# Performance work log

Hardware: AMD Instinct MI355X
Metric: run time of the kernel (lower is better)

## Reference

```python
import jax, jax.numpy as jnp
import numpy as np

N, E, G, D, H, L, IN = 50000, 800000, 16, 64, 4, 4, 7
NEG = 0.2       # LeakyReLU slope (module and GATv2 default)
EPS = 1e-5      # LayerNorm eps


def _lrelu(t):
    return jax.nn.leaky_relu(t, NEG)


def _ln(x, w, b):
    m = x.mean(-1, keepdims=True)
    v = ((x - m) ** 2).mean(-1, keepdims=True)
    return (x - m) * jax.lax.rsqrt(v + EPS) * w + b


def setup_inputs() -> dict:
    key = jax.random.key(0)
    ks = jax.random.split(key, 32)
    p = lambda i, shape: jax.random.normal(ks[i], shape, jnp.float32) * 0.05
    return dict(
        x=jax.random.normal(ks[0], (N, IN), jnp.float32),
        edge_attr=jax.random.normal(ks[1], (E, 3), jnp.float32),
        edge_index=jax.random.randint(ks[2], (2, E), 0, N),
        batch=jnp.sort(jax.random.randint(ks[3], (N,), 0, G)),
        enc_W=p(4, (IN, D)), enc_b=p(5, (D,)),
        Wl=p(6, (L, D, H * D)), bl=p(7, (L, H * D)),
        Wr=p(8, (L, D, H * D)), br=p(9, (L, H * D)),
        We=p(10, (L, 3, H * D)),
        att_w=p(11, (L, H, D)), gat_b=p(12, (L, D)),
        ln1_w=jnp.ones((L, D)), ln1_b=jnp.zeros((L, D)),
        ln2_w=jnp.ones((L, D)), ln2_b=jnp.zeros((L, D)),
        ffn_W1=p(13, (L, D, 2 * D)), ffn_b1=p(14, (L, 2 * D)),
        ffn_W2=p(15, (L, 2 * D, D)), ffn_b2=p(16, (L, D)),
        n2g_W1=p(17, (L, D, D)), n2g_b1=p(18, (L, D)),
        n2g_W2=p(19, (L, D, D)), n2g_b2=p(20, (L, D)),
        g2n_W=p(21, (L, 2 * D, D)), g2n_b=p(22, (L, D)),
        dec_W1=p(23, (D, D)), dec_b1=p(24, (D,)),
        dec_W2=p(25, (D, 2)), dec_b2=p(26, (2,)),
    )


def reference(x, edge_attr, edge_index, batch, enc_W, enc_b, Wl, bl, Wr, br, We,
              att_w, gat_b, ln1_w, ln1_b, ln2_w, ln2_b, ffn_W1, ffn_b1, ffn_W2,
              ffn_b2, n2g_W1, n2g_b1, n2g_W2, n2g_b2, g2n_W, g2n_b,
              dec_W1, dec_b1, dec_W2, dec_b2):
    # add self loops with mean edge_attr fill (PyG GATv2Conv default)
    loops = jnp.arange(N)
    src = jnp.concatenate([edge_index[0], loops])
    dst = jnp.concatenate([edge_index[1], loops])
    ea = jnp.concatenate([edge_attr, jnp.broadcast_to(edge_attr.mean(0), (N, 3))], 0)

    h = x @ enc_W + enc_b  # [N, D]
    for l in range(L):
        # ---- GATv2Conv (heads=H, concat=False -> mean over heads) ----
        xl = (h @ Wl[l] + bl[l]).reshape(N, H, D)   # source transform
        xr = (h @ Wr[l] + br[l]).reshape(N, H, D)   # target transform
        ee = (ea @ We[l]).reshape(-1, H, D)          # edge transform
        s = _lrelu(xl[src] + xr[dst] + ee)           # [Etot, H, D]
        logits = jnp.einsum('ehd,hd->eh', s, att_w[l])
        mx = jax.ops.segment_max(logits, dst, num_segments=N)
        ex = jnp.exp(logits - mx[dst])
        den = jax.ops.segment_sum(ex, dst, num_segments=N)
        alpha = ex / den[dst]                        # segment softmax per dst node
        agg = jax.ops.segment_sum(alpha[..., None] * xl[src], dst, num_segments=N)
        gat_out = agg.mean(1) + gat_b[l]             # [N, D]
        # ---- residual + LN + FFN + LN ----
        h = _ln(h + gat_out, ln1_w[l], ln1_b[l])
        h = _ln(h + _lrelu(h @ ffn_W1[l] + ffn_b1[l]) @ ffn_W2[l] + ffn_b2[l],
                ln2_w[l], ln2_b[l])
        # ---- GlobalContextLayer ----
        lat = _lrelu(h @ n2g_W1[l] + n2g_b1[l]) @ n2g_W2[l] + n2g_b2[l]
        cnt = jnp.maximum(jax.ops.segment_sum(jnp.ones((N,), h.dtype), batch,
                                              num_segments=G), 1.0)
        g_mean = jax.ops.segment_sum(lat, batch, num_segments=G) / cnt[:, None]
        g_max = jax.ops.segment_max(lat, batch, num_segments=G)
        gate = jax.nn.sigmoid(jnp.concatenate([g_mean, g_max], 1) @ g2n_W[l] + g2n_b[l])
        h = h * gate[batch]
    # ---- decoder ----
    return _lrelu(h @ dec_W1 + dec_b1) @ dec_W2 + dec_b2  # [N, 2]
```

## Files before the change

kernel.cpp:

```cpp
#include <hip/hip_runtime.h>

#define DEV __device__ __forceinline__

constexpr int Nn  = 50000;
constexpr int Ee  = 800000;
constexpr int Et  = 850000;
constexpr int Gg  = 16;
constexpr int Dd  = 64;
constexpr int Hh  = 4;
constexpr int Ll  = 4;
constexpr int INd = 7;
constexpr float NEG  = 0.2f;
constexpr float EPSL = 1e-5f;

DEV float lrelu(float x){ return fmaxf(x, NEG*x); }
DEV float wsum64(float v){
  v += __shfl_xor(v,1); v += __shfl_xor(v,2); v += __shfl_xor(v,4);
  v += __shfl_xor(v,8); v += __shfl_xor(v,16); v += __shfl_xor(v,32);
  return v;
}
DEV void atomicMaxF(float* a, float v){
  if (v >= 0.f) atomicMax((int*)a, __float_as_int(v));
  else          atomicMin((unsigned int*)a, __float_as_uint(v));
}
DEV unsigned short f2bf(float f){
  unsigned int u = __float_as_uint(f);
  unsigned int r = (u + 0x7FFFu + ((u >> 16) & 1u)) >> 16;
  return (unsigned short)r;
}
DEV float bf2f(unsigned short b){
  return __uint_as_float(((unsigned int)b) << 16);
}


__global__ void k_init(int* deg, float* g_sum, float* g_max, int* grp_cnt, float* ea_sum){
  int i = blockIdx.x*256 + threadIdx.x;
  if (i < Nn) deg[i] = 0;
  if (i < Gg*Dd){ g_sum[i] = 0.f; g_max[i] = -3.4e38f; }
  if (i < Gg) grp_cnt[i] = 0;
  if (i < 3) ea_sum[i] = 0.f;
}

__global__ void k_eamean(const float* __restrict__ ea, float* __restrict__ ea_sum){
  __shared__ float ps[4][3];
  int tid = threadIdx.x;
  float s0=0.f, s1=0.f, s2=0.f;
  int stride = gridDim.x * blockDim.x;
  for (int i = blockIdx.x*blockDim.x + tid; i < Ee; i += stride){
    s0 += ea[3*i]; s1 += ea[3*i+1]; s2 += ea[3*i+2];
  }
  s0 = wsum64(s0); s1 = wsum64(s1); s2 = wsum64(s2);
  int wid = tid >> 6;
  if ((tid & 63) == 0){ ps[wid][0]=s0; ps[wid][1]=s1; ps[wid][2]=s2; }
  __syncthreads();
  if (tid == 0){
    atomicAdd(ea_sum+0, ps[0][0]+ps[1][0]+ps[2][0]+ps[3][0]);
    atomicAdd(ea_sum+1, ps[0][1]+ps[1][1]+ps[2][1]+ps[3][1]);
    atomicAdd(ea_sum+2, ps[0][2]+ps[1][2]+ps[2][2]+ps[3][2]);
  }
}

__global__ void k_deg(const int* __restrict__ ei_dst, int* __restrict__ deg){
  int e = blockIdx.x*256 + threadIdx.x;
  if (e >= Et) return;
  int dst = (e < Ee) ? ei_dst[e] : (e - Ee);
  atomicAdd(&deg[dst], 1);
}

__global__ void k_bcnt(const int* __restrict__ batch, int* __restrict__ grp_cnt){
  __shared__ int c[Gg];
  if (threadIdx.x < Gg) c[threadIdx.x] = 0;
  __syncthreads();
  int i = blockIdx.x*256 + threadIdx.x;
  if (i < Nn) atomicAdd(&c[batch[i]], 1);
  __syncthreads();
  if (threadIdx.x < Gg && c[threadIdx.x]) atomicAdd(&grp_cnt[threadIdx.x], c[threadIdx.x]);
}

__global__ __launch_bounds__(1024) void k_scan(
    const int* __restrict__ deg, int* __restrict__ indptr, int* __restrict__ fill,
    const float* __restrict__ ea_sum, float* __restrict__ ea_mean)
{
  __shared__ int tot[1024];
  int tid = threadIdx.x;
  if (tid < 3) ea_mean[tid] = ea_sum[tid] * (1.f/(float)Ee);
  constexpr int CH = (Nn + 1023)/1024;
  int b0 = tid*CH;
  int loc[CH];
  int s = 0;
  #pragma unroll
  for (int i=0;i<CH;++i){
    int idx = b0+i;
    int d = (idx < Nn) ? deg[idx] : 0;
    loc[i] = s; s += d;
  }
  tot[tid] = s;
  __syncthreads();
  for (int off=1; off<1024; off<<=1){
    int v = (tid>=off) ? tot[tid-off] : 0;
    __syncthreads();
    tot[tid] += v;
    __syncthreads();
  }
  int base = (tid==0) ? 0 : tot[tid-1];
  #pragma unroll
  for (int i=0;i<CH;++i){
    int idx = b0+i;
    if (idx < Nn){
      int ex = base + loc[i];
      fill[idx] = ex;
      indptr[idx+1] = ex + deg[idx];
    }
  }
  if (tid==0) indptr[0] = 0;
}

__global__ void k_scatter(const int* __restrict__ ei_src, const int* __restrict__ ei_dst,
                          const float* __restrict__ ea, const float* __restrict__ ea_mean,
                          int* __restrict__ fill, float4* __restrict__ meta){
  int e = blockIdx.x*256 + threadIdx.x;
  if (e >= Et) return;
  int src, dst; float a0, a1, a2;
  if (e < Ee){
    src = ei_src[e]; dst = ei_dst[e];
    a0 = ea[3*e]; a1 = ea[3*e+1]; a2 = ea[3*e+2];
  } else {
    src = dst = e - Ee;
    a0 = ea_mean[0]; a1 = ea_mean[1]; a2 = ea_mean[2];
  }
  int pos = atomicAdd(&fill[dst], 1);
  meta[pos] = make_float4(__int_as_float(src), a0, a1, a2);
}

__global__ void k_tw(const float* __restrict__ fW1, const float* __restrict__ gW1,
                     float* __restrict__ fW1T, float* __restrict__ gW1T){
  int i = blockIdx.x*256 + threadIdx.x;
  if (i < Ll*64*128){
    int l = i >> 13, r = (i >> 7) & 63, c = i & 127;
    fW1T[l*8192 + c*64 + r] = fW1[i];
  }
  if (i < Ll*64*64){
    int l = i >> 12, r = (i >> 6) & 63, c = i & 63;
    gW1T[l*4096 + c*64 + r] = gW1[i];
  }
}


__global__ __launch_bounds__(256) void k_enc(
    const float* __restrict__ x, const float* __restrict__ W, const float* __restrict__ b,
    float* __restrict__ h)
{
  int i = blockIdx.x*256 + threadIdx.x;
  if (i >= Nn*Dd) return;
  int n = i >> 6, d = i & 63;
  float s = b[d];
  #pragma unroll
  for (int k=0;k<INd;++k) s = fmaf(x[n*INd+k], W[k*Dd+d], s);
  h[i] = s;
}


__global__ __launch_bounds__(256) void k_xlxr(
    float* __restrict__ h, const float* __restrict__ gate, const int* __restrict__ batch,
    const float* __restrict__ Wl, const float* __restrict__ bl,
    const float* __restrict__ Wr, const float* __restrict__ br,
    unsigned short* __restrict__ xlb, float* __restrict__ xr)
{
  __shared__ float lh[32*68];
  int tid = threadIdx.x;
  int n0 = blockIdx.x * 32;
  for (int r=0; r<8; ++r){
    int idx = r*256 + tid;
    int nl = idx >> 6, d = idx & 63;
    int node = n0 + nl;
    float v = 0.f;
    if (node < Nn){
      v = h[(size_t)node*64 + d];
      if (gate){ v *= gate[batch[node]*64 + d]; h[(size_t)node*64 + d] = v; }
    }
    lh[nl*68 + d] = v;
  }
  __syncthreads();
  int lane = tid & 63;
  int nb = (tid >> 6) * 8;
  int c0 = lane * 8;
  bool isXl = (c0 < 256);
  const float* W; const float* bb; int col;
  if (isXl){ W = Wl; bb = bl; col = c0; }
  else     { W = Wr; bb = br; col = c0 - 256; }
  float4 bA = *reinterpret_cast<const float4*>(bb + col);
  float4 bB = *reinterpret_cast<const float4*>(bb + col + 4);
  float acc[8][8];
  #pragma unroll
  for (int nq=0; nq<8; ++nq){
    acc[nq][0]=bA.x; acc[nq][1]=bA.y; acc[nq][2]=bA.z; acc[nq][3]=bA.w;
    acc[nq][4]=bB.x; acc[nq][5]=bB.y; acc[nq][6]=bB.z; acc[nq][7]=bB.w;
  }
  for (int d=0; d<64; d+=4){
    float4 wA[4], wB[4];
    #pragma unroll
    for (int dq=0; dq<4; ++dq){
      wA[dq] = *reinterpret_cast<const float4*>(W + (d+dq)*256 + col);
      wB[dq] = *reinterpret_cast<const float4*>(W + (d+dq)*256 + col + 4);
    }
    #pragma unroll
    for (int nq=0; nq<8; ++nq){
      float4 hv = *reinterpret_cast<const float4*>(&lh[(nb+nq)*68 + d]);
      #pragma unroll
      for (int dq=0; dq<4; ++dq){
        float hh = (dq==0)? hv.x : (dq==1)? hv.y : (dq==2)? hv.z : hv.w;
        acc[nq][0] = fmaf(hh, wA[dq].x, acc[nq][0]);
        acc[nq][1] = fmaf(hh, wA[dq].y, acc[nq][1]);
        acc[nq][2] = fmaf(hh, wA[dq].z, acc[nq][2]);
        acc[nq][3] = fmaf(hh, wA[dq].w, acc[nq][3]);
        acc[nq][4] = fmaf(hh, wB[dq].x, acc[nq][4]);
        acc[nq][5] = fmaf(hh, wB[dq].y, acc[nq][5]);
        acc[nq][6] = fmaf(hh, wB[dq].z, acc[nq][6]);
        acc[nq][7] = fmaf(hh, wB[dq].w, acc[nq][7]);
      }
    }
  }
  if (isXl){
    #pragma unroll
    for (int nq=0; nq<8; ++nq){
      int node = n0 + nb + nq;
      if (node < Nn){
        uint4 pk;
        pk.x = (unsigned int)f2bf(acc[nq][0]) | ((unsigned int)f2bf(acc[nq][1])<<16);
        pk.y = (unsigned int)f2bf(acc[nq][2]) | ((unsigned int)f2bf(acc[nq][3])<<16);
        pk.z = (unsigned int)f2bf(acc[nq][4]) | ((unsigned int)f2bf(acc[nq][5])<<16);
        pk.w = (unsigned int)f2bf(acc[nq][6]) | ((unsigned int)f2bf(acc[nq][7])<<16);
        *reinterpret_cast<uint4*>(xlb + (size_t)node*256 + col) = pk;
      }
    }
  } else {
    #pragma unroll
    for (int nq=0; nq<8; ++nq){
      int node = n0 + nb + nq;
      if (node < Nn){
        float4 oA = make_float4(acc[nq][0],acc[nq][1],acc[nq][2],acc[nq][3]);
        float4 oB = make_float4(acc[nq][4],acc[nq][5],acc[nq][6],acc[nq][7]);
        *reinterpret_cast<float4*>(xr + (size_t)node*256 + col)     = oA;
        *reinterpret_cast<float4*>(xr + (size_t)node*256 + col + 4) = oB;
      }
    }
  }
}


__global__ __launch_bounds__(256) void k_edge(
    const unsigned short* __restrict__ xlb, const float* __restrict__ xr,
    const int* __restrict__ indptr, const float4* __restrict__ meta,
    const float* __restrict__ We, const float* __restrict__ att,
    float* __restrict__ gat_out)
{
  int lane = threadIdx.x & 63;
  int n = __builtin_amdgcn_readfirstlane(blockIdx.x*4 + (threadIdx.x>>6));
  int coff = (lane>>4)*64 + (lane & 15)*4;

  const float4 xr4 = *reinterpret_cast<const float4*>(xr + (size_t)n*256 + coff);
  const float4 we0 = *reinterpret_cast<const float4*>(We + 0*256 + coff);
  const float4 we1 = *reinterpret_cast<const float4*>(We + 1*256 + coff);
  const float4 we2 = *reinterpret_cast<const float4*>(We + 2*256 + coff);
  const float4 aw  = *reinterpret_cast<const float4*>(att + coff);

  int p0 = __builtin_amdgcn_readfirstlane(indptr[n]);
  int p1 = __builtin_amdgcn_readfirstlane(indptr[n+1]);
  int cnt = p1 - p0;
  const float4* __restrict__ mp = meta + p0;
  int lane7 = lane & 7;
  int ntiles = (cnt + 7) >> 3;

  float den = 0.f, a0c=0.f, a1c=0.f, a2c=0.f, a3c=0.f;

  auto ldm = [&](int t) -> float4 {
    int idx = t*8 + lane7;
    idx = idx < cnt-1 ? idx : cnt-1;
    return mp[idx];
  };
  auto issueXv = [&](const float4& mb, ushort4 (&xv)[8]){
    #pragma unroll
    for (int i=0;i<8;++i){
      int s = __float_as_int(__shfl(mb.x, i));
      xv[i] = *reinterpret_cast<const ushort4*>(xlb + (size_t)s*256 + coff);
    }
  };
  auto compute = [&](const float4& mb, const ushort4 (&xv)[8], int t){
    #pragma unroll
    for (int i=0;i<8;++i){
      float x0 = bf2f(xv[i].x), x1 = bf2f(xv[i].y);
      float x2 = bf2f(xv[i].z), x3 = bf2f(xv[i].w);
      float a0 = __shfl(mb.y, i), a1 = __shfl(mb.z, i), a2 = __shfl(mb.w, i);
      float t0 = fmaf(a0, we0.x, xr4.x); t0 = fmaf(a1, we1.x, t0); t0 = fmaf(a2, we2.x, t0);
      float t1 = fmaf(a0, we0.y, xr4.y); t1 = fmaf(a1, we1.y, t1); t1 = fmaf(a2, we2.y, t1);
      float t2 = fmaf(a0, we0.z, xr4.z); t2 = fmaf(a1, we1.z, t2); t2 = fmaf(a2, we2.z, t2);
      float t3 = fmaf(a0, we0.w, xr4.w); t3 = fmaf(a1, we1.w, t3); t3 = fmaf(a2, we2.w, t3);
      float u0 = lrelu(x0 + t0), u1 = lrelu(x1 + t1);
      float u2 = lrelu(x2 + t2), u3 = lrelu(x3 + t3);
      float part = fmaf(u0, aw.x, fmaf(u1, aw.y, fmaf(u2, aw.z, u3*aw.w)));
      part += __shfl_xor(part,1); part += __shfl_xor(part,2);
      part += __shfl_xor(part,4); part += __shfl_xor(part,8);
      float w = (t*8 + i < cnt) ? __expf(part) : 0.f;
      den += w;
      a0c = fmaf(w, x0, a0c);
      a1c = fmaf(w, x1, a1c);
      a2c = fmaf(w, x2, a2c);
      a3c = fmaf(w, x3, a3c);
    }
  };

  ushort4 xvA[8], xvB[8];
  float4 mCur = ldm(0);
  float4 mNxt = (ntiles > 1) ? ldm(1) : mCur;
  float4 mN2  = mCur;
  issueXv(mCur, xvA);

  int t = 0;
  while (true){
    if (t+2 < ntiles) mN2 = ldm(t+2);
    if (t+1 < ntiles) issueXv(mNxt, xvB);
    compute(mCur, xvA, t);
    if (t+1 >= ntiles) break;
    if (t+3 < ntiles) mCur = ldm(t+3);
    if (t+2 < ntiles) issueXv(mN2, xvA);
    compute(mNxt, xvB, t+1);
    if (t+2 >= ntiles) break;
    float4 tm = mCur; mCur = mN2; mNxt = tm;
    t += 2;
  }

  float inv = 1.f/(den*(float)Hh);
  float s0=a0c*inv, s1=a1c*inv, s2=a2c*inv, s3=a3c*inv;
  s0 += __shfl_xor(s0,16); s0 += __shfl_xor(s0,32);
  s1 += __shfl_xor(s1,16); s1 += __shfl_xor(s1,32);
  s2 += __shfl_xor(s2,16); s2 += __shfl_xor(s2,32);
  s3 += __shfl_xor(s3,16); s3 += __shfl_xor(s3,32);
  int srcl = lane >> 2;
  float w0 = __shfl(s0, srcl), w1 = __shfl(s1, srcl);
  float w2 = __shfl(s2, srcl), w3 = __shfl(s3, srcl);
  int kk = lane & 3;
  float gat = (kk==0)? w0 : (kk==1)? w1 : (kk==2)? w2 : w3;
  gat_out[(size_t)n*64 + lane] = gat;
}


__global__ __launch_bounds__(256) void k_node(
    float* __restrict__ h, const float* __restrict__ gat,
    const float* __restrict__ gatb,
    const float* __restrict__ ln1w, const float* __restrict__ ln1b,
    const float* __restrict__ fW1T, const float* __restrict__ fb1,
    const float* __restrict__ fW2,  const float* __restrict__ fb2,
    const float* __restrict__ ln2w, const float* __restrict__ ln2b,
    const float* __restrict__ gW1T, const float* __restrict__ gb1,
    const float* __restrict__ gW2,  const float* __restrict__ gb2,
    const int* __restrict__ batch, float* __restrict__ g_sum, float* __restrict__ g_max)
{
  __shared__ float4 sW4[4096];
  __shared__ int    sB[256];
  float* sW = reinterpret_cast<float*>(sW4);
  int tid  = threadIdx.x;
  int lane = tid & 63;
  int wv   = tid >> 6;
  int n = blockIdx.x*256 + wv*64 + lane;
  bool valid = n < Nn;
  sB[tid] = valid ? batch[n] : -1;

  {
    const float4* s1 = reinterpret_cast<const float4*>(fW1T);
    const float4* s2 = reinterpret_cast<const float4*>(fW2);
    for (int k=tid; k<2048; k+=256) sW4[k] = s1[k];
    for (int k=tid; k<2048; k+=256) sW4[2048+k] = s2[k];
  }

  float x[64];
  if (valid){
    #pragma unroll
    for (int q=0; q<16; ++q){
      float4 a = *reinterpret_cast<const float4*>(h   + (size_t)n*64 + q*4);
      float4 b = *reinterpret_cast<const float4*>(gat + (size_t)n*64 + q*4);
      float4 g = *reinterpret_cast<const float4*>(gatb + q*4);
      x[q*4+0] = a.x + b.x + g.x;
      x[q*4+1] = a.y + b.y + g.y;
      x[q*4+2] = a.z + b.z + g.z;
      x[q*4+3] = a.w + b.w + g.w;
    }
  } else {
    #pragma unroll
    for (int d=0; d<64; ++d) x[d] = 0.f;
  }

  {
    float s0=0,s1=0,s2=0,s3=0;
    #pragma unroll
    for (int d=0; d<64; d+=4){ s0+=x[d]; s1+=x[d+1]; s2+=x[d+2]; s3+=x[d+3]; }
    float mean = ((s0+s1)+(s2+s3)) * (1.f/64.f);
    float v0=0,v1=0,v2=0,v3=0;
    #pragma unroll
    for (int d=0; d<64; d+=4){
      float a=x[d]-mean, b=x[d+1]-mean, c=x[d+2]-mean, e=x[d+3]-mean;
      v0=fmaf(a,a,v0); v1=fmaf(b,b,v1); v2=fmaf(c,c,v2); v3=fmaf(e,e,v3);
    }
    float rstd = rsqrtf(((v0+v1)+(v2+v3))*(1.f/64.f) + EPSL);
    #pragma unroll
    for (int d=0; d<64; ++d) x[d] = (x[d]-mean)*rstd*ln1w[d] + ln1b[d];
  }
  __syncthreads();

  float o[64];
  #pragma unroll
  for (int j=0; j<64; ++j) o[j] = fb2[j];
  #pragma unroll 2
  for (int c=0; c<128; ++c){
    const float* w1 = sW + c*64;
    float a0=0,a1=0,a2=0,a3=0;
    #pragma unroll
    for (int d=0; d<64; d+=4){
      float4 wv4 = *reinterpret_cast<const float4*>(&w1[d]);
      a0 = fmaf(x[d],   wv4.x, a0);
      a1 = fmaf(x[d+1], wv4.y, a1);
      a2 = fmaf(x[d+2], wv4.z, a2);
      a3 = fmaf(x[d+3], wv4.w, a3);
    }
    float hc = lrelu((a0+a1)+(a2+a3) + fb1[c]);
    const float* w2 = sW + 8192 + c*64;
    #pragma unroll
    for (int j=0; j<64; j+=4){
      float4 wv4 = *reinterpret_cast<const float4*>(&w2[j]);
      o[j]   = fmaf(hc, wv4.x, o[j]);
      o[j+1] = fmaf(hc, wv4.y, o[j+1]);
      o[j+2] = fmaf(hc, wv4.z, o[j+2]);
      o[j+3] = fmaf(hc, wv4.w, o[j+3]);
    }
  }
  __syncthreads();

  {
    const float4* s1 = reinterpret_cast<const float4*>(gW1T);
    const float4* s2 = reinterpret_cast<const float4*>(gW2);
    for (int k=tid; k<1024; k+=256) sW4[k] = s1[k];
    for (int k=tid; k<1024; k+=256) sW4[1024+k] = s2[k];
  }
  {
    #pragma unroll
    for (int d=0; d<64; ++d) x[d] += o[d];
    float s0=0,s1=0,s2=0,s3=0;
    #pragma unroll
    for (int d=0; d<64; d+=4){ s0+=x[d]; s1+=x[d+1]; s2+=x[d+2]; s3+=x[d+3]; }
    float mean = ((s0+s1)+(s2+s3)) * (1.f/64.f);
    float v0=0,v1=0,v2=0,v3=0;
    #pragma unroll
    for (int d=0; d<64; d+=4){
      float a=x[d]-mean, b=x[d+1]-mean, c=x[d+2]-mean, e=x[d+3]-mean;
      v0=fmaf(a,a,v0); v1=fmaf(b,b,v1); v2=fmaf(c,c,v2); v3=fmaf(e,e,v3);
    }
    float rstd = rsqrtf(((v0+v1)+(v2+v3))*(1.f/64.f) + EPSL);
    #pragma unroll
    for (int d=0; d<64; ++d) x[d] = (x[d]-mean)*rstd*ln2w[d] + ln2b[d];
    if (valid){
      #pragma unroll
      for (int q=0; q<16; ++q){
        *reinterpret_cast<float4*>(h + (size_t)n*64 + q*4) =
            make_float4(x[q*4], x[q*4+1], x[q*4+2], x[q*4+3]);
      }
    }
  }
  __syncthreads();

  #pragma unroll
  for (int j=0; j<64; ++j) o[j] = gb2[j];
  #pragma unroll 2
  for (int c=0; c<64; ++c){
    const float* w1 = sW + c*64;
    float a0=0,a1=0,a2=0,a3=0;
    #pragma unroll
    for (int d=0; d<64; d+=4){
      float4 wv4 = *reinterpret_cast<const float4*>(&w1[d]);
      a0 = fmaf(x[d],   wv4.x, a0);
      a1 = fmaf(x[d+1], wv4.y, a1);
      a2 = fmaf(x[d+2], wv4.z, a2);
      a3 = fmaf(x[d+3], wv4.w, a3);
    }
    float uc = lrelu((a0+a1)+(a2+a3) + gb1[c]);
    const float* w2 = sW + 4096 + c*64;
    #pragma unroll
    for (int j=0; j<64; j+=4){
      float4 wv4 = *reinterpret_cast<const float4*>(&w2[j]);
      o[j]   = fmaf(uc, wv4.x, o[j]);
      o[j+1] = fmaf(uc, wv4.y, o[j+1]);
      o[j+2] = fmaf(uc, wv4.z, o[j+2]);
      o[j+3] = fmaf(uc, wv4.w, o[j+3]);
    }
  }
  __syncthreads();

  float* sT = sW + wv*4096;
  #pragma unroll
  for (int j=0; j<64; ++j) sT[j*64 + ((lane+j)&63)] = o[j];
  {
    int cur = -1; float acc = 0.f, mx = -3.4e38f;
    for (int nn=0; nn<64; ++nn){
      int gv = sB[wv*64 + nn];
      float v = sT[lane*64 + ((nn+lane)&63)];
      if (gv != cur){
        if (cur >= 0){
          atomicAdd(g_sum + cur*64 + lane, acc);
          atomicMaxF(g_max + cur*64 + lane, mx);
        }
        cur = gv; acc = 0.f; mx = -3.4e38f;
      }
      if (gv >= 0){ acc += v; mx = fmaxf(mx, v); }
    }
    if (cur >= 0){
      atomicAdd(g_sum + cur*64 + lane, acc);
      atomicMaxF(g_max + cur*64 + lane, mx);
    }
  }
}


__global__ __launch_bounds__(1024) void k_gate(
    float* __restrict__ g_sum, float* __restrict__ g_max, const int* __restrict__ grp_cnt,
    const float* __restrict__ gW, const float* __restrict__ gb, float* __restrict__ gate)
{
  __shared__ float sme[Gg*64];
  __shared__ float smx[Gg*64];
  int tid = threadIdx.x;
  int g = tid >> 6, d = tid & 63;
  float cnt = fmaxf((float)grp_cnt[g], 1.f);
  sme[tid] = g_sum[tid] / cnt;
  smx[tid] = g_max[tid];
  __syncthreads();
  float a = gb[d];
  #pragma unroll
  for (int j=0;j<64;++j){
    a = fmaf(sme[g*64+j], gW[j*64+d],      a);
    a = fmaf(smx[g*64+j], gW[(64+j)*64+d], a);
  }
  gate[tid] = 1.f/(1.f + __expf(-a));
  g_sum[tid] = 0.f;
  g_max[tid] = -3.4e38f;
}


__global__ __launch_bounds__(256) void k_dec(
    const float* __restrict__ h, const float* __restrict__ gate, const int* __restrict__ batch,
    const float* __restrict__ W1, const float* __restrict__ b1,
    const float* __restrict__ W2, const float* __restrict__ b2,
    float* __restrict__ out)
{
  int lane = threadIdx.x & 63;
  int n = __builtin_amdgcn_readfirstlane(blockIdx.x*4 + (threadIdx.x>>6));
  float hv = h[(size_t)n*64 + lane] * gate[batch[n]*64 + lane];
  float hid = b1[lane];
  #pragma unroll
  for (int d2=0; d2<64; ++d2) hid = fmaf(__shfl(hv,d2), W1[d2*64+lane], hid);
  hid = lrelu(hid);
  float r0 = wsum64(hid * W2[lane*2+0]);
  float r1 = wsum64(hid * W2[lane*2+1]);
  if (lane == 0){
    out[(size_t)n*2]   = r0 + b2[0];
    out[(size_t)n*2+1] = r1 + b2[1];
  }
}


extern "C" void kernel_launch(void* const* d_in, const int* in_sizes, int n_in,
                              void* d_out, int out_size, void* d_ws, size_t ws_size,
                              hipStream_t stream) {
  const float* x    = (const float*)d_in[0];
  const float* ea   = (const float*)d_in[1];
  const int*   ei   = (const int*)  d_in[2];
  const int*   bat  = (const int*)  d_in[3];
  const float* encW = (const float*)d_in[4];
  const float* encb = (const float*)d_in[5];
  const float* Wl   = (const float*)d_in[6];
  const float* bl   = (const float*)d_in[7];
  const float* Wr   = (const float*)d_in[8];
  const float* br   = (const float*)d_in[9];
  const float* We   = (const float*)d_in[10];
  const float* attw = (const float*)d_in[11];
  const float* gatb = (const float*)d_in[12];
  const float* ln1w = (const float*)d_in[13];
  const float* ln1b = (const float*)d_in[14];
  const float* ln2w = (const float*)d_in[15];
  const float* ln2b = (const float*)d_in[16];
  const float* fW1  = (const float*)d_in[17];
  const float* fb1  = (const float*)d_in[18];
  const float* fW2  = (const float*)d_in[19];
  const float* fb2  = (const float*)d_in[20];
  const float* gW1  = (const float*)d_in[21];
  const float* gb1  = (const float*)d_in[22];
  const float* gW2  = (const float*)d_in[23];
  const float* gb2  = (const float*)d_in[24];
  const float* g2nW = (const float*)d_in[25];
  const float* g2nb = (const float*)d_in[26];
  const float* dW1  = (const float*)d_in[27];
  const float* db1  = (const float*)d_in[28];
  const float* dW2  = (const float*)d_in[29];
  const float* db2  = (const float*)d_in[30];
  float* out = (float*)d_out;

  char* w = (char*)d_ws;
  float*  h    = (float*)w;  w += (size_t)Nn*64*4;
  unsigned short* xlb = (unsigned short*)w; w += (size_t)Nn*256*2;
  float*  xr   = (float*)w;  w += (size_t)Nn*256*4;
  float4* meta = (float4*)w; w += (size_t)Et*16;
  float*  gatv = (float*)w;  w += (size_t)Nn*64*4;
  float* fW1T = (float*)w; w += (size_t)Ll*128*64*4;
  float* gW1T = (float*)w; w += (size_t)Ll*64*64*4;
  float* gate = (float*)w; w += 1024*4;
  float* gsum = (float*)w; w += 1024*4;
  float* gmax = (float*)w; w += 1024*4;
  float* easum  = (float*)w; w += 16;
  float* eamean = (float*)w; w += 16;
  int* deg    = (int*)w; w += (size_t)Nn*4;
  int* indptr = (int*)w; w += (size_t)(Nn+1)*4;
  int* fill   = (int*)w; w += (size_t)Nn*4;
  int* gcnt   = (int*)w; w += 64;

  const int* ei_src = ei;
  const int* ei_dst = ei + Ee;

  k_init   <<<(Nn+255)/256, 256, 0, stream>>>(deg, gsum, gmax, gcnt, easum);
  k_eamean <<<256, 256, 0, stream>>>(ea, easum);
  k_deg    <<<(Et+255)/256, 256, 0, stream>>>(ei_dst, deg);
  k_bcnt   <<<(Nn+255)/256, 256, 0, stream>>>(bat, gcnt);
  k_scan   <<<1, 1024, 0, stream>>>(deg, indptr, fill, easum, eamean);
  k_scatter<<<(Et+255)/256, 256, 0, stream>>>(ei_src, ei_dst, ea, eamean, fill, meta);
  k_tw     <<<(Ll*64*128+255)/256, 256, 0, stream>>>(fW1, gW1, fW1T, gW1T);
  k_enc    <<<(Nn*64+255)/256, 256, 0, stream>>>(x, encW, encb, h);

  for (int l=0; l<Ll; ++l){
    k_xlxr<<<(Nn+31)/32, 256, 0, stream>>>(h, l ? gate : nullptr, bat,
        Wl + (size_t)l*64*256, bl + (size_t)l*256,
        Wr + (size_t)l*64*256, br + (size_t)l*256, xlb, xr);
    k_edge<<<Nn/4, 256, 0, stream>>>(xlb, xr, indptr, meta,
        We + (size_t)l*3*256, attw + (size_t)l*Hh*64, gatv);
    k_node<<<(Nn+255)/256, 256, 0, stream>>>(h, gatv,
        gatb + (size_t)l*64,
        ln1w + (size_t)l*64, ln1b + (size_t)l*64,
        fW1T + (size_t)l*128*64, fb1 + (size_t)l*128,
        fW2 + (size_t)l*128*64, fb2 + (size_t)l*64,
        ln2w + (size_t)l*64, ln2b + (size_t)l*64,
        gW1T + (size_t)l*64*64, gb1 + (size_t)l*64,
        gW2 + (size_t)l*64*64, gb2 + (size_t)l*64,
        bat, gsum, gmax);
    k_gate<<<1, 1024, 0, stream>>>(gsum, gmax, gcnt,
        g2nW + (size_t)l*128*64, g2nb + (size_t)l*64, gate);
  }

  k_dec<<<Nn/4, 256, 0, stream>>>(h, gate, bat, dW1, db1, dW2, db2, out);
}
```

Baseline: 1.563 ms.

## Split node MLP hidden units across four waves with LDS atomic reduction

```diff
diff --git a/kernel.cpp b/kernel.cpp
--- a/kernel.cpp
+++ b/kernel.cpp
@@ -355,41 +355,35 @@
     const float* __restrict__ gW2,  const float* __restrict__ gb2,
     const int* __restrict__ batch, float* __restrict__ g_sum, float* __restrict__ g_max)
 {
-  __shared__ float4 sW4[4096];
-  __shared__ int    sB[256];
-  float* sW = reinterpret_cast<float*>(sW4);
+  __shared__ float sX[64*64];
+  __shared__ float sO[64*64];
+  __shared__ int   sB[64];
   int tid  = threadIdx.x;
   int lane = tid & 63;
   int wv   = tid >> 6;
-  int n = blockIdx.x*256 + wv*64 + lane;
+  int n = blockIdx.x*64 + lane;
   bool valid = n < Nn;
-  sB[tid] = valid ? batch[n] : -1;
-
-  {
-    const float4* s1 = reinterpret_cast<const float4*>(fW1T);
-    const float4* s2 = reinterpret_cast<const float4*>(fW2);
-    for (int k=tid; k<2048; k+=256) sW4[k] = s1[k];
-    for (int k=tid; k<2048; k+=256) sW4[2048+k] = s2[k];
-  }
+
+  for (int k=tid; k<4096; k+=256) sO[k] = 0.f;
+  if (wv == 0) sB[lane] = valid ? batch[n] : -1;
 
   float x[64];
-  if (valid){
-    #pragma unroll
-    for (int q=0; q<16; ++q){
-      float4 a = *reinterpret_cast<const float4*>(h   + (size_t)n*64 + q*4);
-      float4 b = *reinterpret_cast<const float4*>(gat + (size_t)n*64 + q*4);
-      float4 g = *reinterpret_cast<const float4*>(gatb + q*4);
-      x[q*4+0] = a.x + b.x + g.x;
-      x[q*4+1] = a.y + b.y + g.y;
-      x[q*4+2] = a.z + b.z + g.z;
-      x[q*4+3] = a.w + b.w + g.w;
-    }
-  } else {
-    #pragma unroll
-    for (int d=0; d<64; ++d) x[d] = 0.f;
-  }
-
-  {
+  if (wv == 0){
+    if (valid){
+      #pragma unroll
+      for (int q=0; q<16; ++q){
+        float4 a = *reinterpret_cast<const float4*>(h   + (size_t)n*64 + q*4);
+        float4 b = *reinterpret_cast<const float4*>(gat + (size_t)n*64 + q*4);
+        float4 g = *reinterpret_cast<const float4*>(gatb + q*4);
+        x[q*4+0] = a.x + b.x + g.x;
+        x[q*4+1] = a.y + b.y + g.y;
+        x[q*4+2] = a.z + b.z + g.z;
+        x[q*4+3] = a.w + b.w + g.w;
+      }
+    } else {
+      #pragma unroll
+      for (int d=0; d<64; ++d) x[d] = 0.f;
+    }
     float s0=0,s1=0,s2=0,s3=0;
     #pragma unroll
     for (int d=0; d<64; d+=4){ s0+=x[d]; s1+=x[d+1]; s2+=x[d+2]; s3+=x[d+3]; }
@@ -403,46 +397,53 @@
     float rstd = rsqrtf(((v0+v1)+(v2+v3))*(1.f/64.f) + EPSL);
     #pragma unroll
     for (int d=0; d<64; ++d) x[d] = (x[d]-mean)*rstd*ln1w[d] + ln1b[d];
-  }
-  __syncthreads();
-
-  float o[64];
-  #pragma unroll
-  for (int j=0; j<64; ++j) o[j] = fb2[j];
-  #pragma unroll 2
-  for (int c=0; c<128; ++c){
-    const float* w1 = sW + c*64;
-    float a0=0,a1=0,a2=0,a3=0;
-    #pragma unroll
-    for (int d=0; d<64; d+=4){
-      float4 wv4 = *reinterpret_cast<const float4*>(&w1[d]);
-      a0 = fmaf(x[d],   wv4.x, a0);
-      a1 = fmaf(x[d+1], wv4.y, a1);
-      a2 = fmaf(x[d+2], wv4.z, a2);
-      a3 = fmaf(x[d+3], wv4.w, a3);
-    }
-    float hc = lrelu((a0+a1)+(a2+a3) + fb1[c]);
-    const float* w2 = sW + 8192 + c*64;
-    #pragma unroll
-    for (int j=0; j<64; j+=4){
-      float4 wv4 = *reinterpret_cast<const float4*>(&w2[j]);
-      o[j]   = fmaf(hc, wv4.x, o[j]);
-      o[j+1] = fmaf(hc, wv4.y, o[j+1]);
-      o[j+2] = fmaf(hc, wv4.z, o[j+2]);
-      o[j+3] = fmaf(hc, wv4.w, o[j+3]);
-    }
-  }
-  __syncthreads();
-
+    #pragma unroll
+    for (int j=0; j<64; ++j) sX[lane*64 + ((j+lane)&63)] = x[j];
+  }
+  __syncthreads();
+  if (wv != 0){
+    #pragma unroll
+    for (int j=0; j<64; ++j) x[j] = sX[lane*64 + ((j+lane)&63)];
+  }
+
+  float po[64];
+  if (wv == 0){
+    #pragma unroll
+    for (int j=0; j<64; ++j) po[j] = fb2[j];
+  } else {
+    #pragma unroll
+    for (int j=0; j<64; ++j) po[j] = 0.f;
+  }
   {
-    const float4* s1 = reinterpret_cast<const float4*>(gW1T);
-    const float4* s2 = reinterpret_cast<const float4*>(gW2);
-    for (int k=tid; k<1024; k+=256) sW4[k] = s1[k];
-    for (int k=tid; k<1024; k+=256) sW4[1024+k] = s2[k];
-  }
+    int c0 = wv*32;
+    #pragma unroll 2
+    for (int c=c0; c<c0+32; ++c){
+      const float* __restrict__ w1 = fW1T + c*64;
+      float a0=0,a1=0,a2=0,a3=0;
+      #pragma unroll
+      for (int d=0; d<64; d+=4){
+        a0 = fmaf(x[d],   w1[d],   a0);
+        a1 = fmaf(x[d+1], w1[d+1], a1);
+        a2 = fmaf(x[d+2], w1[d+2], a2);
+        a3 = fmaf(x[d+3], w1[d+3], a3);
+      }
+      float hc = lrelu((a0+a1)+(a2+a3) + fb1[c]);
+      const float* __restrict__ w2 = fW2 + c*64;
+      #pragma unroll
+      for (int j=0; j<64; ++j) po[j] = fmaf(hc, w2[j], po[j]);
+    }
+  }
+  #pragma unroll
+  for (int j=0; j<64; ++j) atomicAdd(&sO[lane*64 + ((j+lane)&63)], po[j]);
+  __syncthreads();
+
+  #pragma unroll
+  for (int j=0; j<64; ++j) po[j] = sO[lane*64 + ((j+lane)&63)];
+  for (int k=tid; k<4096; k+=256) sX[k] = 0.f;
+
   {
     #pragma unroll
-    for (int d=0; d<64; ++d) x[d] += o[d];
+    for (int d=0; d<64; ++d) x[d] += po[d];
     float s0=0,s1=0,s2=0,s3=0;
     #pragma unroll
     for (int d=0; d<64; d+=4){ s0+=x[d]; s1+=x[d+1]; s2+=x[d+2]; s3+=x[d+3]; }
@@ -456,7 +457,7 @@
     float rstd = rsqrtf(((v0+v1)+(v2+v3))*(1.f/64.f) + EPSL);
     #pragma unroll
     for (int d=0; d<64; ++d) x[d] = (x[d]-mean)*rstd*ln2w[d] + ln2b[d];
-    if (valid){
+    if (valid && wv == 0){
       #pragma unroll
       for (int q=0; q<16; ++q){
         *reinterpret_cast<float4*>(h + (size_t)n*64 + q*4) =
@@ -466,41 +467,42 @@
   }
   __syncthreads();
 
-  #pragma unroll
-  for (int j=0; j<64; ++j) o[j] = gb2[j];
-  #pragma unroll 2
-  for (int c=0; c<64; ++c){
-    const float* w1 = sW + c*64;
-    float a0=0,a1=0,a2=0,a3=0;
-    #pragma unroll
-    for (int d=0; d<64; d+=4){
-      float4 wv4 = *reinterpret_cast<const float4*>(&w1[d]);
-      a0 = fmaf(x[d],   wv4.x, a0);
-      a1 = fmaf(x[d+1], wv4.y, a1);
-      a2 = fmaf(x[d+2], wv4.z, a2);
-      a3 = fmaf(x[d+3], wv4.w, a3);
-    }
-    float uc = lrelu((a0+a1)+(a2+a3) + gb1[c]);
-    const float* w2 = sW + 4096 + c*64;
-    #pragma unroll
-    for (int j=0; j<64; j+=4){
-      float4 wv4 = *reinterpret_cast<const float4*>(&w2[j]);
-      o[j]   = fmaf(uc, wv4.x, o[j]);
-      o[j+1] = fmaf(uc, wv4.y, o[j+1]);
-      o[j+2] = fmaf(uc, wv4.z, o[j+2]);
-      o[j+3] = fmaf(uc, wv4.w, o[j+3]);
-    }
-  }
-  __syncthreads();
-
-  float* sT = sW + wv*4096;
-  #pragma unroll
-  for (int j=0; j<64; ++j) sT[j*64 + ((lane+j)&63)] = o[j];
+  if (wv == 0){
+    #pragma unroll
+    for (int j=0; j<64; ++j) po[j] = gb2[j];
+  } else {
+    #pragma unroll
+    for (int j=0; j<64; ++j) po[j] = 0.f;
+  }
+  {
+    int c0 = wv*16;
+    #pragma unroll 2
+    for (int c=c0; c<c0+16; ++c){
+      const float* __restrict__ w1 = gW1T + c*64;
+      float a0=0,a1=0,a2=0,a3=0;
+      #pragma unroll
+      for (int d=0; d<64; d+=4){
+        a0 = fmaf(x[d],   w1[d],   a0);
+        a1 = fmaf(x[d+1], w1[d+1], a1);
+        a2 = fmaf(x[d+2], w1[d+2], a2);
+        a3 = fmaf(x[d+3], w1[d+3], a3);
+      }
+      float uc = lrelu((a0+a1)+(a2+a3) + gb1[c]);
+      const float* __restrict__ w2 = gW2 + c*64;
+      #pragma unroll
+      for (int j=0; j<64; ++j) po[j] = fmaf(uc, w2[j], po[j]);
+    }
+  }
+  #pragma unroll
+  for (int j=0; j<64; ++j) atomicAdd(&sX[lane*64 + ((j+lane)&63)], po[j]);
+  __syncthreads();
+
+  if (wv != 0) return;
   {
     int cur = -1; float acc = 0.f, mx = -3.4e38f;
     for (int nn=0; nn<64; ++nn){
-      int gv = sB[wv*64 + nn];
-      float v = sT[lane*64 + ((nn+lane)&63)];
+      int gv = sB[nn];
+      float v = sX[nn*64 + ((lane+nn)&63)];
       if (gv != cur){
         if (cur >= 0){
           atomicAdd(g_sum + cur*64 + lane, acc);
@@ -636,7 +638,7 @@
         Wr + (size_t)l*64*256, br + (size_t)l*256, xlb, xr);
     k_edge<<<Nn/4, 256, 0, stream>>>(xlb, xr, indptr, meta,
         We + (size_t)l*3*256, attw + (size_t)l*Hh*64, gatv);
-    k_node<<<(Nn+255)/256, 256, 0, stream>>>(h, gatv,
+    k_node<<<(Nn+63)/64, 256, 0, stream>>>(h, gatv,
         gatb + (size_t)l*64,
         ln1w + (size_t)l*64, ln1b + (size_t)l*64,
         fW1T + (size_t)l*128*64, fb1 + (size_t)l*128,
```

Measured after the change: 2.428 ms. 1.55x slower.
